# Optimization experiments

Hardware: AMD Instinct MI355X
Metric: run time of the kernel (lower is better)

Reference implementation:

```python
import jax, jax.numpy as jnp
import numpy as np

N, E = 50000, 800000
IN_CH, HID, OUT, EDIM = 151, 128, 51, 51


def setup_inputs() -> dict:
    key = jax.random.key(0)
    ks = jax.random.split(key, 10)
    def w(k, shape, fan_in):
        return jax.random.normal(k, shape, jnp.float32) * (1.0 / np.sqrt(fan_in))
    return {
        "x": jax.random.normal(ks[0], (N, IN_CH), jnp.float32),
        "edge_attr": jax.random.normal(ks[1], (E, EDIM), jnp.float32),
        "W_edge0": w(ks[2], (EDIM, IN_CH), EDIM),
        "b_edge0": jnp.zeros((IN_CH,), jnp.float32),
        "W0": w(ks[3], (IN_CH, HID), IN_CH),
        "b0": jnp.zeros((HID,), jnp.float32),
        "W_edge1": w(ks[4], (EDIM, HID), EDIM),
        "b_edge1": jnp.zeros((HID,), jnp.float32),
        "W1": w(ks[5], (HID, HID), HID),
        "b1": jnp.zeros((HID,), jnp.float32),
        "W_out": w(ks[6], (HID, OUT), HID),
        "b_out": jnp.zeros((OUT,), jnp.float32),
        "edge_index": jax.random.randint(ks[7], (2, E), 0, N, jnp.int32),
    }


def gtn_layer(x, src, dst, edge_attr, W_e, b_e, W, b):
    # message: x_j + Linear(edge_attr);  aggr='add' scatter to dst.
    eat = edge_attr @ W_e + b_e                                # [E, in_ch]
    msgs = x[src] + eat                                        # gather + add
    agg = jax.ops.segment_sum(msgs, dst, num_segments=x.shape[0])
    # self-loops carry zero edge_attr -> transformed attr == bias b_e,
    # so their message is x + b_e (equivalent to concatenating N self-loop edges).
    agg = agg + x + b_e
    return agg @ W + b                                         # self.linear


def reference(x, edge_attr, W_edge0, b_edge0, W0, b0, W_edge1, b_edge1, W1, b1, W_out, b_out, edge_index):
    src, dst = edge_index[0], edge_index[1]
    h = gtn_layer(x, src, dst, edge_attr, W_edge0, b_edge0, W0, b0)   # [N, HID]
    h = gtn_layer(h, src, dst, edge_attr, W_edge1, b_edge1, W1, b1)   # [N, HID]
    # global_mean_pool with batch=arange(N) is identity (one node per graph)
    return h @ W_out + b_out                                          # [N, OUT]
```

## Files before the change

kernel.cpp:

```cpp
#include <hip/hip_runtime.h>

#define N_NODES 50000
#define N_EDGES 800000
#define IN_CH   151
#define HID     128
#define OUT_CH  51
#define EDIM    51
#define WP      64
#define LSTR    68
#define NBLK    ((N_NODES + 255) / 256)

static __device__ __forceinline__ unsigned int f2bf(float f) {
    union { float f; unsigned int u; } v; v.f = f;
    unsigned int r = v.u + 0x7FFF + ((v.u >> 16) & 1);
    return r >> 16;
}
static __device__ __forceinline__ float bflo(unsigned int u) {
    return __uint_as_float(u << 16);
}
static __device__ __forceinline__ float bfhi(unsigned int u) {
    return __uint_as_float(u & 0xFFFF0000u);
}

__global__ void kw1(const float* __restrict__ We0, const float* __restrict__ W0,
                    const float* __restrict__ be0, const float* __restrict__ W1,
                    const float* __restrict__ Wout,
                    float* __restrict__ M0, float* __restrict__ c0, float* __restrict__ Wc) {
    int t = blockIdx.x * blockDim.x + threadIdx.x;
    if (t < 51 * 128) {
        int i = t / 128, j = t % 128;
        float a = 0.f;
        for (int k = 0; k < IN_CH; ++k) a += We0[i * IN_CH + k] * W0[k * HID + j];
        M0[t] = a;
    } else if (t < 51 * 128 + 128) {
        int j = t - 51 * 128;
        float a = 0.f;
        for (int k = 0; k < IN_CH; ++k) a += be0[k] * W0[k * HID + j];
        c0[j] = a;
    } else if (t < 51 * 128 + 128 + 128 * WP) {
        int u = t - (51 * 128 + 128);
        int i = u / WP, j = u % WP;
        float a = 0.f;
        if (j < OUT_CH)
            for (int k = 0; k < HID; ++k) a += W1[i * HID + k] * Wout[k * OUT_CH + j];
        Wc[i * WP + j] = a;
    }
}

__global__ void kw2(const float* __restrict__ We1, const float* __restrict__ be1,
                    const float* __restrict__ b1, const float* __restrict__ Wout,
                    const float* __restrict__ bout, const float* __restrict__ Wc,
                    float* __restrict__ Mc, float* __restrict__ cc, float* __restrict__ dd) {
    int t = blockIdx.x * blockDim.x + threadIdx.x;
    if (t < 51 * WP) {
        int i = t / WP, j = t % WP;
        float a = 0.f;
        if (j < OUT_CH)
            for (int k = 0; k < HID; ++k) a += We1[i * HID + k] * Wc[k * WP + j];
        Mc[t] = a;
    } else if (t < 51 * WP + 51) {
        int j = t - 51 * WP;
        float a = 0.f;
        for (int k = 0; k < HID; ++k) a += be1[k] * Wc[k * WP + j];
        cc[j] = a;
    } else if (t < 51 * WP + 102) {
        int j = t - (51 * WP + 51);
        float a = 0.f;
        for (int k = 0; k < HID; ++k) a += b1[k] * Wout[k * OUT_CH + j];
        dd[j] = a + bout[j];
    }
}

__global__ void k_hist(const int* __restrict__ ei, int* __restrict__ deg) {
    int e = blockIdx.x * 256 + threadIdx.x;
    if (e >= N_EDGES) return;
    atomicAdd(&deg[ei[N_EDGES + e]], 1);
}

__global__ void scan1(const int* __restrict__ deg, int* __restrict__ blksum) {
    __shared__ int lds[256];
    int i = blockIdx.x * 256 + threadIdx.x;
    lds[threadIdx.x] = (i < N_NODES) ? deg[i] : 0;
    __syncthreads();
    for (int s = 128; s > 0; s >>= 1) {
        if (threadIdx.x < s) lds[threadIdx.x] += lds[threadIdx.x + s];
        __syncthreads();
    }
    if (threadIdx.x == 0) blksum[blockIdx.x] = lds[0];
}

__global__ void scan2(const int* __restrict__ blksum, int* __restrict__ blkoff) {
    __shared__ int lds[256];
    int v = (threadIdx.x < NBLK) ? blksum[threadIdx.x] : 0;
    lds[threadIdx.x] = v;
    __syncthreads();
    for (int s = 1; s < 256; s <<= 1) {
        int t = (threadIdx.x >= s) ? lds[threadIdx.x - s] : 0;
        __syncthreads();
        lds[threadIdx.x] += t;
        __syncthreads();
    }
    if (threadIdx.x < NBLK) blkoff[threadIdx.x] = lds[threadIdx.x] - v;
}

__global__ void scan3(const int* __restrict__ deg, const int* __restrict__ blkoff,
                      int* __restrict__ row_start, int* __restrict__ cursor) {
    __shared__ int lds[256];
    int i = blockIdx.x * 256 + threadIdx.x;
    int v = (i < N_NODES) ? deg[i] : 0;
    lds[threadIdx.x] = v;
    __syncthreads();
    for (int s = 1; s < 256; s <<= 1) {
        int t = (threadIdx.x >= s) ? lds[threadIdx.x - s] : 0;
        __syncthreads();
        lds[threadIdx.x] += t;
        __syncthreads();
    }
    if (i < N_NODES) {
        int ex = blkoff[blockIdx.x] + lds[threadIdx.x] - v;
        row_start[i] = ex;
        cursor[i] = ex;
    }
    if (blockIdx.x == 0 && threadIdx.x == 0) row_start[N_NODES] = N_EDGES;
}

__global__ void k_fill(const int* __restrict__ ei, int* __restrict__ cursor,
                       int* __restrict__ eid_sorted, int* __restrict__ src_sorted) {
    int e = blockIdx.x * 256 + threadIdx.x;
    if (e >= N_EDGES) return;
    int dst = ei[N_EDGES + e];
    int pos = atomicAdd(&cursor[dst], 1);
    eid_sorted[pos] = e;
    src_sorted[pos] = ei[e];
}

__global__ void k_agg_S(const float* __restrict__ ea, const int* __restrict__ eid_sorted,
                        const int* __restrict__ row_start, float* __restrict__ S) {
    int n = blockIdx.x * 4 + (threadIdx.x >> 6);
    if (n >= N_NODES) return;
    int lane = threadIdx.x & 63;
    int n0 = row_start[n], n1 = row_start[n + 1];
    float acc = 0.f;
    bool act = lane < EDIM;
    for (int base = n0; base < n1; base += 64) {
        int cnt = min(64, n1 - base);
        int eid_l = (base + lane < n1) ? eid_sorted[base + lane] : 0;
        int t = 0;
        for (; t + 8 <= cnt; t += 8) {
            int e0 = __shfl(eid_l, t),     e1 = __shfl(eid_l, t + 1);
            int e2 = __shfl(eid_l, t + 2), e3 = __shfl(eid_l, t + 3);
            int e4 = __shfl(eid_l, t + 4), e5 = __shfl(eid_l, t + 5);
            int e6 = __shfl(eid_l, t + 6), e7 = __shfl(eid_l, t + 7);
            float v0 = act ? ea[(size_t)e0 * EDIM + lane] : 0.f;
            float v1 = act ? ea[(size_t)e1 * EDIM + lane] : 0.f;
            float v2 = act ? ea[(size_t)e2 * EDIM + lane] : 0.f;
            float v3 = act ? ea[(size_t)e3 * EDIM + lane] : 0.f;
            float v4 = act ? ea[(size_t)e4 * EDIM + lane] : 0.f;
            float v5 = act ? ea[(size_t)e5 * EDIM + lane] : 0.f;
            float v6 = act ? ea[(size_t)e6 * EDIM + lane] : 0.f;
            float v7 = act ? ea[(size_t)e7 * EDIM + lane] : 0.f;
            acc += ((v0 + v1) + (v2 + v3)) + ((v4 + v5) + (v6 + v7));
        }
        for (; t < cnt; ++t) {
            int e0 = __shfl(eid_l, t);
            if (act) acc += ea[(size_t)e0 * EDIM + lane];
        }
    }
    if (act) S[(size_t)n * EDIM + lane] = acc;
}

__global__ void k_agg_h(const unsigned int* __restrict__ yb, const int* __restrict__ src_sorted,
                        const int* __restrict__ row_start, float* __restrict__ hacc) {
    int n = blockIdx.x * 4 + (threadIdx.x >> 6);
    if (n >= N_NODES) return;
    int lane = threadIdx.x & 63;
    int n0 = row_start[n], n1 = row_start[n + 1];
    float2 acc = make_float2(0.f, 0.f);
    for (int base = n0; base < n1; base += 64) {
        int cnt = min(64, n1 - base);
        int s_l = (base + lane < n1) ? src_sorted[base + lane] : 0;
        int t = 0;
        for (; t + 8 <= cnt; t += 8) {
            int s0 = __shfl(s_l, t),     s1 = __shfl(s_l, t + 1);
            int s2 = __shfl(s_l, t + 2), s3 = __shfl(s_l, t + 3);
            int s4 = __shfl(s_l, t + 4), s5 = __shfl(s_l, t + 5);
            int s6 = __shfl(s_l, t + 6), s7 = __shfl(s_l, t + 7);
            unsigned int v0 = yb[(size_t)s0 * 64 + lane];
            unsigned int v1 = yb[(size_t)s1 * 64 + lane];
            unsigned int v2 = yb[(size_t)s2 * 64 + lane];
            unsigned int v3 = yb[(size_t)s3 * 64 + lane];
            unsigned int v4 = yb[(size_t)s4 * 64 + lane];
            unsigned int v5 = yb[(size_t)s5 * 64 + lane];
            unsigned int v6 = yb[(size_t)s6 * 64 + lane];
            unsigned int v7 = yb[(size_t)s7 * 64 + lane];
            acc.x += ((bflo(v0) + bflo(v1)) + (bflo(v2) + bflo(v3)))
                   + ((bflo(v4) + bflo(v5)) + (bflo(v6) + bflo(v7)));
            acc.y += ((bfhi(v0) + bfhi(v1)) + (bfhi(v2) + bfhi(v3)))
                   + ((bfhi(v4) + bfhi(v5)) + (bfhi(v6) + bfhi(v7)));
        }
        for (; t < cnt; ++t) {
            int s0 = __shfl(s_l, t);
            unsigned int v0 = yb[(size_t)s0 * 64 + lane];
            acc.x += bflo(v0); acc.y += bfhi(v0);
        }
    }
    float2* hp = (float2*)(hacc + (size_t)n * HID) + lane;
    float2 old = *hp;
    old.x += acc.x; old.y += acc.y;
    *hp = old;
}

__global__ void k_agg_out(const unsigned short* __restrict__ wb, const int* __restrict__ src_sorted,
                          const int* __restrict__ row_start, float* __restrict__ out) {
    int n = blockIdx.x * 4 + (threadIdx.x >> 6);
    if (n >= N_NODES) return;
    int lane = threadIdx.x & 63;
    int n0 = row_start[n], n1 = row_start[n + 1];
    float acc = 0.f;
    bool act = lane < OUT_CH;
    for (int base = n0; base < n1; base += 64) {
        int cnt = min(64, n1 - base);
        int s_l = (base + lane < n1) ? src_sorted[base + lane] : 0;
        int t = 0;
        for (; t + 8 <= cnt; t += 8) {
            int s0 = __shfl(s_l, t),     s1 = __shfl(s_l, t + 1);
            int s2 = __shfl(s_l, t + 2), s3 = __shfl(s_l, t + 3);
            int s4 = __shfl(s_l, t + 4), s5 = __shfl(s_l, t + 5);
            int s6 = __shfl(s_l, t + 6), s7 = __shfl(s_l, t + 7);
            unsigned int v0 = act ? wb[(size_t)s0 * WP + lane] : 0u;
            unsigned int v1 = act ? wb[(size_t)s1 * WP + lane] : 0u;
            unsigned int v2 = act ? wb[(size_t)s2 * WP + lane] : 0u;
            unsigned int v3 = act ? wb[(size_t)s3 * WP + lane] : 0u;
            unsigned int v4 = act ? wb[(size_t)s4 * WP + lane] : 0u;
            unsigned int v5 = act ? wb[(size_t)s5 * WP + lane] : 0u;
            unsigned int v6 = act ? wb[(size_t)s6 * WP + lane] : 0u;
            unsigned int v7 = act ? wb[(size_t)s7 * WP + lane] : 0u;
            acc += ((bflo(v0) + bflo(v1)) + (bflo(v2) + bflo(v3)))
                 + ((bflo(v4) + bflo(v5)) + (bflo(v6) + bflo(v7)));
        }
        for (; t < cnt; ++t) {
            int s0 = __shfl(s_l, t);
            if (act) acc += bflo((unsigned int)wb[(size_t)s0 * WP + lane]);
        }
    }
    if (act) out[(size_t)n * OUT_CH + lane] += acc;
}

__global__ __launch_bounds__(256, 4) void k_layer0(
        const float* __restrict__ x, const float* __restrict__ W0,
        const float* __restrict__ b0, const float* __restrict__ S,
        const int* __restrict__ deg, const float* __restrict__ M0,
        const float* __restrict__ c0,
        unsigned int* __restrict__ yb, float* __restrict__ hacc) {
    __shared__ float aT[64 * LSTR];
    int tid = threadIdx.x;
    int r_base = blockIdx.x * 64;
    int cg = tid & 15, rg = tid >> 4;
    int c = cg * 8, r0 = rg * 4;

    float4 accA[4], accB[4];
#pragma unroll
    for (int i = 0; i < 4; ++i) {
        accA[i] = make_float4(0.f, 0.f, 0.f, 0.f);
        accB[i] = make_float4(0.f, 0.f, 0.f, 0.f);
    }

    for (int p = 0; p < 3; ++p) {
        int koff = p * 64;
        int chunk = min(64, IN_CH - koff);
        __syncthreads();
        for (int idx = tid; idx < 64 * 64; idx += 256) {
            int r = idx >> 6, kk = idx & 63;
            if (kk >= chunk) continue;
            int row = r_base + r;
            aT[kk * LSTR + r] = (row < N_NODES) ? x[(size_t)row * IN_CH + koff + kk] : 0.f;
        }
        __syncthreads();
#pragma unroll 4
        for (int kk = 0; kk < chunk; ++kk) {
            int k = koff + kk;
            float4 wv0 = *(const float4*)(W0 + k * HID + c);
            float4 wv1 = *(const float4*)(W0 + k * HID + c + 4);
            float4 a0 = *(const float4*)(&aT[kk * LSTR + r0]);
            float ar[4] = {a0.x, a0.y, a0.z, a0.w};
#pragma unroll
            for (int i = 0; i < 4; ++i) {
                accA[i].x += ar[i] * wv0.x; accA[i].y += ar[i] * wv0.y;
                accA[i].z += ar[i] * wv0.z; accA[i].w += ar[i] * wv0.w;
                accB[i].x += ar[i] * wv1.x; accB[i].y += ar[i] * wv1.y;
                accB[i].z += ar[i] * wv1.z; accB[i].w += ar[i] * wv1.w;
            }
        }
    }

#pragma unroll
    for (int i = 0; i < 4; ++i) {
        int row = r_base + r0 + i;
        if (row < N_NODES) {
            uint4 pk;
            pk.x = f2bf(accA[i].x) | (f2bf(accA[i].y) << 16);
            pk.y = f2bf(accA[i].z) | (f2bf(accA[i].w) << 16);
            pk.z = f2bf(accB[i].x) | (f2bf(accB[i].y) << 16);
            pk.w = f2bf(accB[i].z) | (f2bf(accB[i].w) << 16);
            *(uint4*)(yb + (size_t)row * 64 + (c >> 1)) = pk;
        }
    }

    __syncthreads();
    for (int idx = tid; idx < 64 * 64; idx += 256) {
        int r = idx >> 6, kk = idx & 63;
        if (kk >= EDIM) continue;
        int row = r_base + r;
        aT[kk * LSTR + r] = (row < N_NODES) ? S[(size_t)row * EDIM + kk] : 0.f;
    }
    __syncthreads();
#pragma unroll 4
    for (int kk = 0; kk < EDIM; ++kk) {
        float4 wv0 = *(const float4*)(M0 + kk * HID + c);
        float4 wv1 = *(const float4*)(M0 + kk * HID + c + 4);
        float4 a0 = *(const float4*)(&aT[kk * LSTR + r0]);
        float ar[4] = {a0.x, a0.y, a0.z, a0.w};
#pragma unroll
        for (int i = 0; i < 4; ++i) {
            accA[i].x += ar[i] * wv0.x; accA[i].y += ar[i] * wv0.y;
            accA[i].z += ar[i] * wv0.z; accA[i].w += ar[i] * wv0.w;
            accB[i].x += ar[i] * wv1.x; accB[i].y += ar[i] * wv1.y;
            accB[i].z += ar[i] * wv1.z; accB[i].w += ar[i] * wv1.w;
        }
    }

    float4 cv0 = *(const float4*)(c0 + c);
    float4 cv1 = *(const float4*)(c0 + c + 4);
    float4 bv0 = *(const float4*)(b0 + c);
    float4 bv1 = *(const float4*)(b0 + c + 4);
#pragma unroll
    for (int i = 0; i < 4; ++i) {
        int row = r_base + r0 + i;
        if (row < N_NODES) {
            float d1 = (float)(deg[row] + 1);
            float4 vA = accA[i], vB = accB[i];
            vA.x += d1 * cv0.x + bv0.x; vA.y += d1 * cv0.y + bv0.y;
            vA.z += d1 * cv0.z + bv0.z; vA.w += d1 * cv0.w + bv0.w;
            vB.x += d1 * cv1.x + bv1.x; vB.y += d1 * cv1.y + bv1.y;
            vB.z += d1 * cv1.z + bv1.z; vB.w += d1 * cv1.w + bv1.w;
            *(float4*)(hacc + (size_t)row * HID + c) = vA;
            *(float4*)(hacc + (size_t)row * HID + c + 4) = vB;
        }
    }
}

__global__ __launch_bounds__(256, 4) void k_layer1(
        const float* __restrict__ hacc, const float* __restrict__ Wc,
        const float* __restrict__ S, const int* __restrict__ deg,
        const float* __restrict__ Mc, const float* __restrict__ cc,
        const float* __restrict__ dd,
        unsigned int* __restrict__ wb, float* __restrict__ out) {
    __shared__ float aT[64 * LSTR];
    int tid = threadIdx.x;
    int r_base = blockIdx.x * 64;
    int cg = tid & 15, rg = tid >> 4;
    int c = cg * 4, r0 = rg * 4;

    float4 acc[4];
#pragma unroll
    for (int i = 0; i < 4; ++i) acc[i] = make_float4(0.f, 0.f, 0.f, 0.f);

    for (int p = 0; p < 2; ++p) {
        int koff = p * 64;
        __syncthreads();
        for (int idx = tid; idx < 64 * 64; idx += 256) {
            int r = idx >> 6, kk = idx & 63;
            int row = r_base + r;
            aT[kk * LSTR + r] = (row < N_NODES) ? hacc[(size_t)row * HID + koff + kk] : 0.f;
        }
        __syncthreads();
#pragma unroll 4
        for (int kk = 0; kk < 64; ++kk) {
            int k = koff + kk;
            float4 wv = *(const float4*)(Wc + k * WP + c);
            float4 a0 = *(const float4*)(&aT[kk * LSTR + r0]);
            float ar[4] = {a0.x, a0.y, a0.z, a0.w};
#pragma unroll
            for (int i = 0; i < 4; ++i) {
                acc[i].x += ar[i] * wv.x; acc[i].y += ar[i] * wv.y;
                acc[i].z += ar[i] * wv.z; acc[i].w += ar[i] * wv.w;
            }
        }
    }

#pragma unroll
    for (int i = 0; i < 4; ++i) {
        int row = r_base + r0 + i;
        if (row < N_NODES) {
            uint2 pk;
            pk.x = f2bf(acc[i].x) | (f2bf(acc[i].y) << 16);
            pk.y = f2bf(acc[i].z) | (f2bf(acc[i].w) << 16);
            *(uint2*)(wb + (size_t)row * 32 + (c >> 1)) = pk;
        }
    }

    __syncthreads();
    for (int idx = tid; idx < 64 * 64; idx += 256) {
        int r = idx >> 6, kk = idx & 63;
        if (kk >= EDIM) continue;
        int row = r_base + r;
        aT[kk * LSTR + r] = (row < N_NODES) ? S[(size_t)row * EDIM + kk] : 0.f;
    }
    __syncthreads();
#pragma unroll 4
    for (int kk = 0; kk < EDIM; ++kk) {
        float4 wv = *(const float4*)(Mc + kk * WP + c);
        float4 a0 = *(const float4*)(&aT[kk * LSTR + r0]);
        float ar[4] = {a0.x, a0.y, a0.z, a0.w};
#pragma unroll
        for (int i = 0; i < 4; ++i) {
            acc[i].x += ar[i] * wv.x; acc[i].y += ar[i] * wv.y;
            acc[i].z += ar[i] * wv.z; acc[i].w += ar[i] * wv.w;
        }
    }

    if (c < OUT_CH) {
        float cv[4], dv[4];
#pragma unroll
        for (int j = 0; j < 4; ++j) {
            int col = c + j;
            cv[j] = (col < OUT_CH) ? cc[col] : 0.f;
            dv[j] = (col < OUT_CH) ? dd[col] : 0.f;
        }
#pragma unroll
        for (int i = 0; i < 4; ++i) {
            int row = r_base + r0 + i;
            if (row < N_NODES) {
                float d1 = (float)(deg[row] + 1);
                const float* ap = (const float*)&acc[i];
#pragma unroll
                for (int j = 0; j < 4; ++j) {
                    int col = c + j;
                    if (col < OUT_CH)
                        out[(size_t)row * OUT_CH + col] = ap[j] + d1 * cv[j] + dv[j];
                }
            }
        }
    }
}

extern "C" void kernel_launch(void* const* d_in, const int* in_sizes, int n_in,
                              void* d_out, int out_size, void* d_ws, size_t ws_size,
                              hipStream_t stream) {
    const float* x    = (const float*)d_in[0];
    const float* ea   = (const float*)d_in[1];
    const float* We0  = (const float*)d_in[2];
    const float* be0  = (const float*)d_in[3];
    const float* W0   = (const float*)d_in[4];
    const float* b0   = (const float*)d_in[5];
    const float* We1  = (const float*)d_in[6];
    const float* be1  = (const float*)d_in[7];
    const float* W1   = (const float*)d_in[8];
    const float* b1   = (const float*)d_in[9];
    const float* Wout = (const float*)d_in[10];
    const float* bout = (const float*)d_in[11];
    const int*   ei   = (const int*)d_in[12];
    float* out = (float*)d_out;

    char* p = (char*)d_ws;
    auto alloc = [&](size_t bytes) {
        char* r = p;
        p += (bytes + 255) & ~(size_t)255;
        return r;
    };
    float* S         = (float*)alloc((size_t)N_NODES * EDIM * 4);
    int*   deg       = (int*)  alloc((size_t)N_NODES * 4);
    int*   row_start = (int*)  alloc((size_t)(N_NODES + 1) * 4);
    int*   cursor    = (int*)  alloc((size_t)N_NODES * 4);
    int*   blksum    = (int*)  alloc((size_t)NBLK * 4);
    int*   blkoff    = (int*)  alloc((size_t)NBLK * 4);
    int*   eid_srt   = (int*)  alloc((size_t)N_EDGES * 4);
    int*   src_srt   = (int*)  alloc((size_t)N_EDGES * 4);
    unsigned int* yb = (unsigned int*)alloc((size_t)N_NODES * 64 * 4);
    float* hacc      = (float*)alloc((size_t)N_NODES * HID * 4);
    unsigned int* wb = (unsigned int*)alloc((size_t)N_NODES * 32 * 4);
    float* M0        = (float*)alloc(51 * 128 * 4);
    float* c0        = (float*)alloc(128 * 4);
    float* Wc        = (float*)alloc(128 * WP * 4);
    float* Mc        = (float*)alloc(51 * WP * 4);
    float* cc        = (float*)alloc(51 * 4);
    float* dd        = (float*)alloc(51 * 4);

    hipMemsetAsync(deg, 0, (size_t)N_NODES * 4, stream);

    kw1<<<(51 * 128 + 128 + 128 * WP + 255) / 256, 256, 0, stream>>>(
        We0, W0, be0, W1, Wout, M0, c0, Wc);
    kw2<<<(51 * WP + 102 + 255) / 256, 256, 0, stream>>>(
        We1, be1, b1, Wout, bout, Wc, Mc, cc, dd);

    k_hist<<<(N_EDGES + 255) / 256, 256, 0, stream>>>(ei, deg);
    scan1<<<NBLK, 256, 0, stream>>>(deg, blksum);
    scan2<<<1, 256, 0, stream>>>(blksum, blkoff);
    scan3<<<NBLK, 256, 0, stream>>>(deg, blkoff, row_start, cursor);
    k_fill<<<(N_EDGES + 255) / 256, 256, 0, stream>>>(ei, cursor, eid_srt, src_srt);

    k_agg_S<<<(N_NODES + 3) / 4, 256, 0, stream>>>(ea, eid_srt, row_start, S);

    k_layer0<<<(N_NODES + 63) / 64, 256, 0, stream>>>(x, W0, b0, S, deg, M0, c0, yb, hacc);
    k_agg_h<<<(N_NODES + 3) / 4, 256, 0, stream>>>(yb, src_srt, row_start, hacc);

    k_layer1<<<(N_NODES + 63) / 64, 256, 0, stream>>>(hacc, Wc, S, deg, Mc, cc, dd, wb, out);
    k_agg_out<<<(N_NODES + 3) / 4, 256, 0, stream>>>((const unsigned short*)wb, src_srt, row_start, out);
}
```

Baseline: 610.9 us.

## Merge CSR-build kernels, pack src/eid pairs, and vectorize gathers with uint4

Folds the degree histogram into the weight-precompute kernel, scan1 into the second weight kernel, and scan2 into scan3, so fewer kernels are launched. The separate sorted src and edge-id arrays become one interleaved int2 array. The neighbor gathers in k_agg_h and k_agg_out now use 16-byte uint4 loads, with several edges processed per wavefront in parallel, followed by a cross-lane shuffle reduction. This is meant to cut launch overhead and the number of memory transactions, at the cost of redundant per-block scan work and extra shuffle reductions.

```diff
diff --git a/kernel.cpp b/kernel.cpp
--- a/kernel.cpp
+++ b/kernel.cpp
@@ -9,6 +9,11 @@
 #define WP      64
 #define LSTR    68
 #define NBLK    ((N_NODES + 255) / 256)
+#define EBLK    ((N_EDGES + 255) / 256)
+#define KW1_T   (51 * 128 + 128 + 128 * WP)
+#define KW1_B   ((KW1_T + 255) / 256)
+#define KW2_T   (51 * WP + 102)
+#define KW2_B   ((KW2_T + 255) / 256)
 
 static __device__ __forceinline__ unsigned int f2bf(float f) {
     union { float f; unsigned int u; } v; v.f = f;
@@ -22,11 +27,18 @@
     return __uint_as_float(u & 0xFFFF0000u);
 }
 
-__global__ void kw1(const float* __restrict__ We0, const float* __restrict__ W0,
-                    const float* __restrict__ be0, const float* __restrict__ W1,
-                    const float* __restrict__ Wout,
-                    float* __restrict__ M0, float* __restrict__ c0, float* __restrict__ Wc) {
-    int t = blockIdx.x * blockDim.x + threadIdx.x;
+__global__ void k_hist_kw1(const int* __restrict__ ei, int* __restrict__ deg,
+                           const float* __restrict__ We0, const float* __restrict__ W0,
+                           const float* __restrict__ be0, const float* __restrict__ W1,
+                           const float* __restrict__ Wout,
+                           float* __restrict__ M0, float* __restrict__ c0,
+                           float* __restrict__ Wc) {
+    if (blockIdx.x < EBLK) {
+        int e = blockIdx.x * 256 + threadIdx.x;
+        if (e < N_EDGES) atomicAdd(&deg[ei[N_EDGES + e]], 1);
+        return;
+    }
+    int t = (blockIdx.x - EBLK) * 256 + threadIdx.x;
     if (t < 51 * 128) {
         int i = t / 128, j = t % 128;
         float a = 0.f;
@@ -47,11 +59,25 @@
     }
 }
 
-__global__ void kw2(const float* __restrict__ We1, const float* __restrict__ be1,
-                    const float* __restrict__ b1, const float* __restrict__ Wout,
-                    const float* __restrict__ bout, const float* __restrict__ Wc,
-                    float* __restrict__ Mc, float* __restrict__ cc, float* __restrict__ dd) {
-    int t = blockIdx.x * blockDim.x + threadIdx.x;
+__global__ void k_scan1_kw2(const int* __restrict__ deg, int* __restrict__ blksum,
+                            const float* __restrict__ We1, const float* __restrict__ be1,
+                            const float* __restrict__ b1, const float* __restrict__ Wout,
+                            const float* __restrict__ bout, const float* __restrict__ Wc,
+                            float* __restrict__ Mc, float* __restrict__ cc,
+                            float* __restrict__ dd) {
+    if (blockIdx.x < NBLK) {
+        __shared__ int lds[256];
+        int i = blockIdx.x * 256 + threadIdx.x;
+        lds[threadIdx.x] = (i < N_NODES) ? deg[i] : 0;
+        __syncthreads();
+        for (int s = 128; s > 0; s >>= 1) {
+            if (threadIdx.x < s) lds[threadIdx.x] += lds[threadIdx.x + s];
+            __syncthreads();
+        }
+        if (threadIdx.x == 0) blksum[blockIdx.x] = lds[0];
+        return;
+    }
+    int t = (blockIdx.x - NBLK) * 256 + threadIdx.x;
     if (t < 51 * WP) {
         int i = t / WP, j = t % WP;
         float a = 0.f;
@@ -71,70 +97,52 @@
     }
 }
 
-__global__ void k_hist(const int* __restrict__ ei, int* __restrict__ deg) {
+__global__ void k_scan3m(const int* __restrict__ deg, const int* __restrict__ blksum,
+                         int* __restrict__ row_start, int* __restrict__ cursor) {
+    __shared__ int lds[256];
+    __shared__ int s_off;
+    int tid = threadIdx.x;
+    int v2 = (tid < NBLK) ? blksum[tid] : 0;
+    lds[tid] = v2;
+    __syncthreads();
+    for (int s = 1; s < 256; s <<= 1) {
+        int t = (tid >= s) ? lds[tid - s] : 0;
+        __syncthreads();
+        lds[tid] += t;
+        __syncthreads();
+    }
+    if (tid == 0) s_off = (blockIdx.x == 0) ? 0 : lds[blockIdx.x - 1];
+    __syncthreads();
+    int boff = s_off;
+    int i = blockIdx.x * 256 + tid;
+    int v = (i < N_NODES) ? deg[i] : 0;
+    lds[tid] = v;
+    __syncthreads();
+    for (int s = 1; s < 256; s <<= 1) {
+        int t = (tid >= s) ? lds[tid - s] : 0;
+        __syncthreads();
+        lds[tid] += t;
+        __syncthreads();
+    }
+    if (i < N_NODES) {
+        int ex = boff + lds[tid] - v;
+        row_start[i] = ex;
+        cursor[i] = ex;
+    }
+    if (blockIdx.x == 0 && tid == 0) row_start[N_NODES] = N_EDGES;
+}
+
+__global__ void k_fill(const int* __restrict__ ei, int* __restrict__ cursor,
+                       int2* __restrict__ pairs) {
     int e = blockIdx.x * 256 + threadIdx.x;
     if (e >= N_EDGES) return;
-    atomicAdd(&deg[ei[N_EDGES + e]], 1);
-}
-
-__global__ void scan1(const int* __restrict__ deg, int* __restrict__ blksum) {
-    __shared__ int lds[256];
-    int i = blockIdx.x * 256 + threadIdx.x;
-    lds[threadIdx.x] = (i < N_NODES) ? deg[i] : 0;
-    __syncthreads();
-    for (int s = 128; s > 0; s >>= 1) {
-        if (threadIdx.x < s) lds[threadIdx.x] += lds[threadIdx.x + s];
-        __syncthreads();
-    }
-    if (threadIdx.x == 0) blksum[blockIdx.x] = lds[0];
-}
-
-__global__ void scan2(const int* __restrict__ blksum, int* __restrict__ blkoff) {
-    __shared__ int lds[256];
-    int v = (threadIdx.x < NBLK) ? blksum[threadIdx.x] : 0;
-    lds[threadIdx.x] = v;
-    __syncthreads();
-    for (int s = 1; s < 256; s <<= 1) {
-        int t = (threadIdx.x >= s) ? lds[threadIdx.x - s] : 0;
-        __syncthreads();
-        lds[threadIdx.x] += t;
-        __syncthreads();
-    }
-    if (threadIdx.x < NBLK) blkoff[threadIdx.x] = lds[threadIdx.x] - v;
-}
-
-__global__ void scan3(const int* __restrict__ deg, const int* __restrict__ blkoff,
-                      int* __restrict__ row_start, int* __restrict__ cursor) {
-    __shared__ int lds[256];
-    int i = blockIdx.x * 256 + threadIdx.x;
-    int v = (i < N_NODES) ? deg[i] : 0;
-    lds[threadIdx.x] = v;
-    __syncthreads();
-    for (int s = 1; s < 256; s <<= 1) {
-        int t = (threadIdx.x >= s) ? lds[threadIdx.x - s] : 0;
-        __syncthreads();
-        lds[threadIdx.x] += t;
-        __syncthreads();
-    }
-    if (i < N_NODES) {
-        int ex = blkoff[blockIdx.x] + lds[threadIdx.x] - v;
-        row_start[i] = ex;
-        cursor[i] = ex;
-    }
-    if (blockIdx.x == 0 && threadIdx.x == 0) row_start[N_NODES] = N_EDGES;
-}
-
-__global__ void k_fill(const int* __restrict__ ei, int* __restrict__ cursor,
-                       int* __restrict__ eid_sorted, int* __restrict__ src_sorted) {
-    int e = blockIdx.x * 256 + threadIdx.x;
-    if (e >= N_EDGES) return;
+    int src = ei[e];
     int dst = ei[N_EDGES + e];
     int pos = atomicAdd(&cursor[dst], 1);
-    eid_sorted[pos] = e;
-    src_sorted[pos] = ei[e];
-}
-
-__global__ void k_agg_S(const float* __restrict__ ea, const int* __restrict__ eid_sorted,
+    pairs[pos] = make_int2(src, e);
+}
+
+__global__ void k_agg_S(const float* __restrict__ ea, const int2* __restrict__ pairs,
                         const int* __restrict__ row_start, float* __restrict__ S) {
     int n = blockIdx.x * 4 + (threadIdx.x >> 6);
     if (n >= N_NODES) return;
@@ -144,7 +152,7 @@
     bool act = lane < EDIM;
     for (int base = n0; base < n1; base += 64) {
         int cnt = min(64, n1 - base);
-        int eid_l = (base + lane < n1) ? eid_sorted[base + lane] : 0;
+        int eid_l = (base + lane < n1) ? pairs[base + lane].y : 0;
         int t = 0;
         for (; t + 8 <= cnt; t += 8) {
             int e0 = __shfl(eid_l, t),     e1 = __shfl(eid_l, t + 1);
@@ -169,81 +177,85 @@
     if (act) S[(size_t)n * EDIM + lane] = acc;
 }
 
-__global__ void k_agg_h(const unsigned int* __restrict__ yb, const int* __restrict__ src_sorted,
+__global__ void k_agg_h(const uint4* __restrict__ yb4, const int2* __restrict__ pairs,
                         const int* __restrict__ row_start, float* __restrict__ hacc) {
     int n = blockIdx.x * 4 + (threadIdx.x >> 6);
     if (n >= N_NODES) return;
     int lane = threadIdx.x & 63;
+    int g = lane >> 4, s = lane & 15;
     int n0 = row_start[n], n1 = row_start[n + 1];
-    float2 acc = make_float2(0.f, 0.f);
+    float acc[8];
+#pragma unroll
+    for (int j = 0; j < 8; ++j) acc[j] = 0.f;
     for (int base = n0; base < n1; base += 64) {
         int cnt = min(64, n1 - base);
-        int s_l = (base + lane < n1) ? src_sorted[base + lane] : 0;
-        int t = 0;
-        for (; t + 8 <= cnt; t += 8) {
-            int s0 = __shfl(s_l, t),     s1 = __shfl(s_l, t + 1);
-            int s2 = __shfl(s_l, t + 2), s3 = __shfl(s_l, t + 3);
-            int s4 = __shfl(s_l, t + 4), s5 = __shfl(s_l, t + 5);
-            int s6 = __shfl(s_l, t + 6), s7 = __shfl(s_l, t + 7);
-            unsigned int v0 = yb[(size_t)s0 * 64 + lane];
-            unsigned int v1 = yb[(size_t)s1 * 64 + lane];
-            unsigned int v2 = yb[(size_t)s2 * 64 + lane];
-            unsigned int v3 = yb[(size_t)s3 * 64 + lane];
-            unsigned int v4 = yb[(size_t)s4 * 64 + lane];
-            unsigned int v5 = yb[(size_t)s5 * 64 + lane];
-            unsigned int v6 = yb[(size_t)s6 * 64 + lane];
-            unsigned int v7 = yb[(size_t)s7 * 64 + lane];
-            acc.x += ((bflo(v0) + bflo(v1)) + (bflo(v2) + bflo(v3)))
-                   + ((bflo(v4) + bflo(v5)) + (bflo(v6) + bflo(v7)));
-            acc.y += ((bfhi(v0) + bfhi(v1)) + (bfhi(v2) + bfhi(v3)))
-                   + ((bfhi(v4) + bfhi(v5)) + (bfhi(v6) + bfhi(v7)));
-        }
-        for (; t < cnt; ++t) {
-            int s0 = __shfl(s_l, t);
-            unsigned int v0 = yb[(size_t)s0 * 64 + lane];
-            acc.x += bflo(v0); acc.y += bfhi(v0);
-        }
-    }
-    float2* hp = (float2*)(hacc + (size_t)n * HID) + lane;
-    float2 old = *hp;
-    old.x += acc.x; old.y += acc.y;
-    *hp = old;
-}
-
-__global__ void k_agg_out(const unsigned short* __restrict__ wb, const int* __restrict__ src_sorted,
+        int s_l = (base + lane < n1) ? pairs[base + lane].x : 0;
+        for (int t = 0; t < cnt; t += 4) {
+            int idx = t + g;
+            bool ok = idx < cnt;
+            int srcn = __shfl(s_l, ok ? idx : 0);
+            if (ok) {
+                uint4 v = yb4[(size_t)srcn * 16 + s];
+                acc[0] += bflo(v.x); acc[1] += bfhi(v.x);
+                acc[2] += bflo(v.y); acc[3] += bfhi(v.y);
+                acc[4] += bflo(v.z); acc[5] += bfhi(v.z);
+                acc[6] += bflo(v.w); acc[7] += bfhi(v.w);
+            }
+        }
+    }
+#pragma unroll
+    for (int j = 0; j < 8; ++j) {
+        acc[j] += __shfl_xor(acc[j], 16);
+        acc[j] += __shfl_xor(acc[j], 32);
+    }
+    if (lane < 16) {
+        float4* hp = (float4*)(hacc + (size_t)n * HID + lane * 8);
+        float4 a = hp[0], b = hp[1];
+        a.x += acc[0]; a.y += acc[1]; a.z += acc[2]; a.w += acc[3];
+        b.x += acc[4]; b.y += acc[5]; b.z += acc[6]; b.w += acc[7];
+        hp[0] = a; hp[1] = b;
+    }
+}
+
+__global__ void k_agg_out(const uint4* __restrict__ wb4, const int2* __restrict__ pairs,
                           const int* __restrict__ row_start, float* __restrict__ out) {
     int n = blockIdx.x * 4 + (threadIdx.x >> 6);
     if (n >= N_NODES) return;
     int lane = threadIdx.x & 63;
+    int g = lane >> 3, s = lane & 7;
     int n0 = row_start[n], n1 = row_start[n + 1];
-    float acc = 0.f;
-    bool act = lane < OUT_CH;
+    float acc[8];
+#pragma unroll
+    for (int j = 0; j < 8; ++j) acc[j] = 0.f;
     for (int base = n0; base < n1; base += 64) {
         int cnt = min(64, n1 - base);
-        int s_l = (base + lane < n1) ? src_sorted[base + lane] : 0;
-        int t = 0;
-        for (; t + 8 <= cnt; t += 8) {
-            int s0 = __shfl(s_l, t),     s1 = __shfl(s_l, t + 1);
-            int s2 = __shfl(s_l, t + 2), s3 = __shfl(s_l, t + 3);
-            int s4 = __shfl(s_l, t + 4), s5 = __shfl(s_l, t + 5);
-            int s6 = __shfl(s_l, t + 6), s7 = __shfl(s_l, t + 7);
-            unsigned int v0 = act ? wb[(size_t)s0 * WP + lane] : 0u;
-            unsigned int v1 = act ? wb[(size_t)s1 * WP + lane] : 0u;
-            unsigned int v2 = act ? wb[(size_t)s2 * WP + lane] : 0u;
-            unsigned int v3 = act ? wb[(size_t)s3 * WP + lane] : 0u;
-            unsigned int v4 = act ? wb[(size_t)s4 * WP + lane] : 0u;
-            unsigned int v5 = act ? wb[(size_t)s5 * WP + lane] : 0u;
-            unsigned int v6 = act ? wb[(size_t)s6 * WP + lane] : 0u;
-            unsigned int v7 = act ? wb[(size_t)s7 * WP + lane] : 0u;
-            acc += ((bflo(v0) + bflo(v1)) + (bflo(v2) + bflo(v3)))
-                 + ((bflo(v4) + bflo(v5)) + (bflo(v6) + bflo(v7)));
-        }
-        for (; t < cnt; ++t) {
-            int s0 = __shfl(s_l, t);
-            if (act) acc += bflo((unsigned int)wb[(size_t)s0 * WP + lane]);
-        }
-    }
-    if (act) out[(size_t)n * OUT_CH + lane] += acc;
+        int s_l = (base + lane < n1) ? pairs[base + lane].x : 0;
+        for (int t = 0; t < cnt; t += 8) {
+            int idx = t + g;
+            bool ok = idx < cnt;
+            int srcn = __shfl(s_l, ok ? idx : 0);
+            if (ok) {
+                uint4 v = wb4[(size_t)srcn * 8 + s];
+                acc[0] += bflo(v.x); acc[1] += bfhi(v.x);
+                acc[2] += bflo(v.y); acc[3] += bfhi(v.y);
+                acc[4] += bflo(v.z); acc[5] += bfhi(v.z);
+                acc[6] += bflo(v.w); acc[7] += bfhi(v.w);
+            }
+        }
+    }
+#pragma unroll
+    for (int j = 0; j < 8; ++j) {
+        acc[j] += __shfl_xor(acc[j], 8);
+        acc[j] += __shfl_xor(acc[j], 16);
+        acc[j] += __shfl_xor(acc[j], 32);
+    }
+    if (lane < 8) {
+#pragma unroll
+        for (int j = 0; j < 8; ++j) {
+            int ch = lane * 8 + j;
+            if (ch < OUT_CH) out[(size_t)n * OUT_CH + ch] += acc[j];
+        }
+    }
 }
 
 __global__ __launch_bounds__(256, 4) void k_layer0(
@@ -473,9 +485,7 @@
     int*   row_start = (int*)  alloc((size_t)(N_NODES + 1) * 4);
     int*   cursor    = (int*)  alloc((size_t)N_NODES * 4);
     int*   blksum    = (int*)  alloc((size_t)NBLK * 4);
-    int*   blkoff    = (int*)  alloc((size_t)NBLK * 4);
-    int*   eid_srt   = (int*)  alloc((size_t)N_EDGES * 4);
-    int*   src_srt   = (int*)  alloc((size_t)N_EDGES * 4);
+    int2*  pairs     = (int2*) alloc((size_t)N_EDGES * 8);
     unsigned int* yb = (unsigned int*)alloc((size_t)N_NODES * 64 * 4);
     float* hacc      = (float*)alloc((size_t)N_NODES * HID * 4);
     unsigned int* wb = (unsigned int*)alloc((size_t)N_NODES * 32 * 4);
@@ -488,22 +498,17 @@
 
     hipMemsetAsync(deg, 0, (size_t)N_NODES * 4, stream);
 
-    kw1<<<(51 * 128 + 128 + 128 * WP + 255) / 256, 256, 0, stream>>>(
-        We0, W0, be0, W1, Wout, M0, c0, Wc);
-    kw2<<<(51 * WP + 102 + 255) / 256, 256, 0, stream>>>(
-        We1, be1, b1, Wout, bout, Wc, Mc, cc, dd);
-
-    k_hist<<<(N_EDGES + 255) / 256, 256, 0, stream>>>(ei, deg);
-    scan1<<<NBLK, 256, 0, stream>>>(deg, blksum);
-    scan2<<<1, 256, 0, stream>>>(blksum, blkoff);
-    scan3<<<NBLK, 256, 0, stream>>>(deg, blkoff, row_start, cursor);
-    k_fill<<<(N_EDGES + 255) / 256, 256, 0, stream>>>(ei, cursor, eid_srt, src_srt);
-
-    k_agg_S<<<(N_NODES + 3) / 4, 256, 0, stream>>>(ea, eid_srt, row_start, S);
+    k_hist_kw1<<<EBLK + KW1_B, 256, 0, stream>>>(ei, deg, We0, W0, be0, W1, Wout, M0, c0, Wc);
+    k_scan1_kw2<<<NBLK + KW2_B, 256, 0, stream>>>(deg, blksum, We1, be1, b1, Wout, bout,
+                                                  Wc, Mc, cc, dd);
+    k_scan3m<<<NBLK, 256, 0, stream>>>(deg, blksum, row_start, cursor);
+    k_fill<<<EBLK, 256, 0, stream>>>(ei, cursor, pairs);
+
+    k_agg_S<<<(N_NODES + 3) / 4, 256, 0, stream>>>(ea, pairs, row_start, S);
 
     k_layer0<<<(N_NODES + 63) / 64, 256, 0, stream>>>(x, W0, b0, S, deg, M0, c0, yb, hacc);
-    k_agg_h<<<(N_NODES + 3) / 4, 256, 0, stream>>>(yb, src_srt, row_start, hacc);
+    k_agg_h<<<(N_NODES + 3) / 4, 256, 0, stream>>>((const uint4*)yb, pairs, row_start, hacc);
 
     k_layer1<<<(N_NODES + 63) / 64, 256, 0, stream>>>(hacc, Wc, S, deg, Mc, cc, dd, wb, out);
-    k_agg_out<<<(N_NODES + 3) / 4, 256, 0, stream>>>((const unsigned short*)wb, src_srt, row_start, out);
-}
+    k_agg_out<<<(N_NODES + 3) / 4, 256, 0, stream>>>((const uint4*)wb, pairs, row_start, out);
+}
```

New measurement: 589.6 us. 3.5% less time.
